# Kernel optimization log

Measured on AMD Instinct MI355X. Metric: run time of the kernel, lower is better.

Reference implementation:

```python
import jax, jax.numpy as jnp
import numpy as np
from jax import lax

B = 32; C_IN = 3; HW = 64
CL1_F = 64; CL1_K = 5
V = 1024
CL2_F = 128; CL2_K = 16
CL3_F = 256; CL3_K = 16
FC1_F = 512; FC2_F = 10
FC1_IN = CL3_F * (V // 16)  # 16384


def _sym_laplacian(k, v):
    # symmetric, spectral norm < 1 (mimics rescaled Laplacian 2L/lmax - I spectrum)
    a = jax.random.normal(k, (v, v), jnp.float32) / np.float32(np.sqrt(v))
    return (a + a.T) * jnp.float32(0.3)


def setup_inputs():
    key = jax.random.key(0)
    ks = jax.random.split(key, 10)
    def n(k, shape, s):
        return jax.random.normal(k, shape, jnp.float32) * jnp.float32(s)
    x = jax.random.normal(ks[0], (B, C_IN, HW, HW), jnp.float32)
    conv1_w = n(ks[1], (CL1_F, C_IN, CL1_K, CL1_K), 0.05)
    conv1_b = jnp.zeros((CL1_F,), jnp.float32)
    L1 = _sym_laplacian(ks[2], V)
    L2 = _sym_laplacian(ks[3], V // 4)
    g = HW // 2  # pooled grid side = 32
    ii, jj = jnp.meshgrid(jnp.arange(g), jnp.arange(g), indexing='ij')
    node_index = jnp.stack([ii.reshape(-1), jj.reshape(-1)], axis=1).astype(jnp.int32)  # [V,2]
    perm = jnp.arange(V, dtype=jnp.int32)
    k2_w = n(ks[4], (CL2_F, CL1_F * CL2_K), 0.04)
    k2_b = jnp.zeros((CL2_F,), jnp.float32)
    k3_w = n(ks[5], (CL3_F, CL2_F * CL3_K), 0.03)
    k3_b = jnp.zeros((CL3_F,), jnp.float32)
    fc1_w = n(ks[6], (FC1_F, FC1_IN), 0.01)
    fc1_b = jnp.zeros((FC1_F,), jnp.float32)
    fc2_w = n(ks[7], (FC2_F, FC1_F), 0.05)
    fc2_b = jnp.zeros((FC2_F,), jnp.float32)
    return {"x": x, "conv1_w": conv1_w, "conv1_b": conv1_b, "L1": L1, "L2": L2,
            "node_index": node_index, "perm": perm,
            "k2_w": k2_w, "k2_b": k2_b, "k3_w": k3_w, "k3_b": k3_b,
            "fc1_w": fc1_w, "fc1_b": fc1_b, "fc2_w": fc2_w, "fc2_b": fc2_b}


def _graph_conv(x, L, W, b, K):
    # x: (B, C, V). Chebyshev basis T_k(L) x, then linear over (C*K).
    Bb, C, Vv = x.shape
    x0 = jnp.transpose(x, (2, 1, 0)).reshape(Vv, C * Bb)  # [V, C*B]
    xs = [x0, L @ x0]
    for _ in range(K - 2):
        xs.append(2.0 * (L @ xs[-1]) - xs[-2])
    xk = jnp.stack(xs, axis=0).reshape(K, Vv, C, Bb)  # [K,V,C,B]
    xk = jnp.transpose(xk, (3, 1, 2, 0)).reshape(Bb * Vv, C * K)  # [B*V, C*K]
    out = xk @ W.T + b  # [B*V, Fout]
    return jnp.transpose(out.reshape(Bb, Vv, -1), (0, 2, 1))  # (B, Fout, V)


def reference(x, conv1_w, conv1_b, L1, L2, node_index, perm,
              k2_w, k2_b, k3_w, k3_b, fc1_w, fc1_b, fc2_w, fc2_b):
    pad = (CL1_K - 1) // 2
    y = lax.conv_general_dilated(x, conv1_w, (1, 1), [(pad, pad), (pad, pad)],
                                 dimension_numbers=('NCHW', 'OIHW', 'NCHW'))
    y = jax.nn.relu(y + conv1_b[None, :, None, None])
    Bb, C, H, Wd = y.shape
    y = y.reshape(Bb, C, H // 2, 2, Wd // 2, 2).max(axis=(3, 5))  # MaxPool2d(2,2)
    y = y[:, :, node_index[:, 0], node_index[:, 1]]  # (B, C, V)
    y = y[:, :, perm]
    # BatchNorm1d(affine=False), training-mode batch stats, biased variance
    mean = y.mean(axis=(0, 2), keepdims=True)
    var = y.var(axis=(0, 2), keepdims=True)
    y = (y - mean) * lax.rsqrt(var + 1e-5)
    y = jax.nn.relu(_graph_conv(y, L1, k2_w, k2_b, CL2_K))
    y = y.reshape(Bb, CL2_F, -1, 4).max(axis=-1)  # Graph_MaxPool(4)
    y = jax.nn.relu(_graph_conv(y, L2, k3_w, k3_b, CL3_K))
    y = y.reshape(Bb, CL3_F, -1, 4).max(axis=-1)
    y = y.reshape(Bb, FC1_IN)
    y = jax.nn.relu(y @ fc1_w.T + fc1_b)  # dropout p=0 -> identity
    return y @ fc2_w.T + fc2_b
```

## Files before the change

### kernel.cpp

```cpp
#include <hip/hip_runtime.h>
#include <hip/hip_bf16.h>

#define BB 32
#define C_IN 3
#define HW 64
#define V1 1024
#define CL2_F 128
#define V2 256
#define CL3_F 256
#define FC1_IN 16384

typedef unsigned short ushortT;
typedef __attribute__((ext_vector_type(8))) short bf16x8;
typedef __attribute__((ext_vector_type(8))) unsigned short u16x8;
typedef __attribute__((ext_vector_type(4))) float f32x4;

__device__ __forceinline__ float bfu2f(unsigned short u) {
  union { unsigned int i; float f; } x; x.i = ((unsigned)u) << 16; return x.f;
}
__device__ __forceinline__ unsigned short f2bf(float v) {
  union { float f; unsigned int i; } x; x.f = v;
  unsigned r = x.i + 0x7FFFu + ((x.i >> 16) & 1u);
  return (unsigned short)(r >> 16);
}
__device__ __forceinline__ void gload16(const ushortT* g, ushortT* l) {
  __builtin_amdgcn_global_load_lds((const __attribute__((address_space(1))) void*)g,
                                   (__attribute__((address_space(3))) void*)l, 16, 0, 0);
}

__global__ __launch_bounds__(256) void conv_pool_k(const float* __restrict__ x,
                                                   const float* __restrict__ w,
                                                   const float* __restrict__ bias,
                                                   float* __restrict__ P) {
  __shared__ float xs[3][7][72];
  __shared__ float wl[64][76];
  const int b = blockIdx.x >> 5, ph = blockIdx.x & 31;
  const int t = threadIdx.x;
  for (int i = t; i < 64 * 75; i += 256) wl[i / 75][i % 75] = w[i];
  for (int i = t; i < 3 * 7 * 72; i += 256) {
    int col = i % 72, rr = (i / 72) % 7, ci = i / (72 * 7);
    int ih = 2 * ph - 2 + rr, iw = col - 2;
    float v = 0.f;
    if (ih >= 0 && ih < HW && iw >= 0 && iw < HW)
      v = x[((b * 3 + ci) * HW + ih) * HW + iw];
    xs[ci][rr][col] = v;
  }
  __syncthreads();
  const int co = t >> 2, pq = t & 3;
  float acc[8][2][2];
#pragma unroll
  for (int i = 0; i < 8; ++i)
#pragma unroll
    for (int a = 0; a < 2; ++a)
#pragma unroll
      for (int d = 0; d < 2; ++d) acc[i][a][d] = 0.f;
  for (int ci = 0; ci < 3; ++ci) {
#pragma unroll
    for (int kh = 0; kh < 5; ++kh) {
      float w5[5];
#pragma unroll
      for (int j = 0; j < 5; ++j) w5[j] = wl[co][ci * 25 + kh * 5 + j];
#pragma unroll
      for (int dy = 0; dy < 2; ++dy) {
        const int r = kh + dy;
        float in[20];
#pragma unroll
        for (int q4 = 0; q4 < 5; ++q4) {
          float4 v4 = *(const float4*)&xs[ci][r][16 * pq + q4 * 4];
          in[q4 * 4 + 0] = v4.x; in[q4 * 4 + 1] = v4.y;
          in[q4 * 4 + 2] = v4.z; in[q4 * 4 + 3] = v4.w;
        }
#pragma unroll
        for (int i = 0; i < 8; ++i)
#pragma unroll
          for (int dx = 0; dx < 2; ++dx)
#pragma unroll
            for (int kw = 0; kw < 5; ++kw)
              acc[i][dy][dx] += w5[kw] * in[2 * i + dx + kw];
      }
    }
  }
  const float bv = bias[co];
#pragma unroll
  for (int i = 0; i < 8; ++i) {
    float m = fmaxf(fmaxf(acc[i][0][0], acc[i][0][1]), fmaxf(acc[i][1][0], acc[i][1][1]));
    P[((size_t)(b * 64 + co) << 10) + (ph << 5) + pq * 8 + i] = fmaxf(m + bv, 0.f);
  }
}

__global__ __launch_bounds__(256) void bn_part_k(const float* __restrict__ P,
                                                 float* __restrict__ buf) {
  int c = blockIdx.x, s = blockIdx.y;
  float s1 = 0.f, s2 = 0.f;
  for (int i = threadIdx.x; i < 4096; i += 256) {
    int b = s * 4 + (i >> 10), p = i & 1023;
    float v = P[((size_t)(b * 64 + c) << 10) + p];
    s1 += v; s2 += v * v;
  }
#pragma unroll
  for (int o = 32; o > 0; o >>= 1) { s1 += __shfl_down(s1, o); s2 += __shfl_down(s2, o); }
  __shared__ float sh[2][4];
  int wid = threadIdx.x >> 6;
  if ((threadIdx.x & 63) == 0) { sh[0][wid] = s1; sh[1][wid] = s2; }
  __syncthreads();
  if (threadIdx.x == 0) {
    buf[c * 8 + s] = sh[0][0] + sh[0][1] + sh[0][2] + sh[0][3];
    buf[512 + c * 8 + s] = sh[1][0] + sh[1][1] + sh[1][2] + sh[1][3];
  }
}
__global__ __launch_bounds__(64) void bn_comb_k(float* __restrict__ buf) {
  int c = threadIdx.x;
  float s1 = 0.f, s2 = 0.f;
#pragma unroll
  for (int s = 0; s < 8; ++s) { s1 += buf[c * 8 + s]; s2 += buf[512 + c * 8 + s]; }
  float mean = s1 / 32768.f;
  float var = s2 / 32768.f - mean * mean;
  buf[1024 + c] = mean;
  buf[1088 + c] = rsqrtf(var + 1e-5f);
}

__global__ __launch_bounds__(256) void build_x0_k(const float* __restrict__ P,
                                                  const float* __restrict__ buf,
                                                  const int* __restrict__ ni,
                                                  const int* __restrict__ perm,
                                                  ushortT* __restrict__ PGh,
                                                  ushortT* __restrict__ PGl,
                                                  ushortT* __restrict__ CW0) {
  __shared__ float vals[64][33];
  __shared__ int qv[32];
  const int b = blockIdx.x >> 5, vc = blockIdx.x & 31;
  const int t = threadIdx.x;
  if (t < 32) {
    int pv = perm[vc * 32 + t];
    qv[t] = ni[2 * pv] * 32 + ni[2 * pv + 1];
  }
  __syncthreads();
  {
    int c = t & 63, vh = t >> 6;
    float mean = buf[1024 + c], rstd = buf[1088 + c];
    const float* pc = &P[((size_t)(b * 64 + c)) << 10];
#pragma unroll
    for (int j = 0; j < 8; ++j) {
      int vl = vh * 8 + j;
      vals[c][vl] = (pc[qv[vl]] - mean) * rstd;
    }
  }
  __syncthreads();
  {
    int c = t & 63, vo = t >> 6;
    u16x8 h8, l8;
#pragma unroll
    for (int j = 0; j < 8; ++j) {
      float f = vals[c][vo * 8 + j];
      unsigned short h = f2bf(f);
      h8[j] = h; l8[j] = f2bf(f - bfu2f(h));
    }
    size_t base = ((size_t)(vc * 4 + vo) * 2048 + b * 64 + c) * 8;
    *(u16x8*)&PGh[base] = h8;
    *(u16x8*)&PGl[base] = l8;
  }
  {
    int co = t & 7, vl = t >> 3;
    u16x8 h8;
#pragma unroll
    for (int j = 0; j < 8; ++j) h8[j] = f2bf(vals[co * 8 + j][vl]);
    *(u16x8*)&CW0[((size_t)co * 32768 + b * 1024 + vc * 32 + vl) * 8] = h8;
  }
}

__global__ __launch_bounds__(256) void lsplit_k(const float* __restrict__ L,
                                                ushortT* __restrict__ Lh,
                                                ushortT* __restrict__ Ll, int V) {
  int id = blockIdx.x * 256 + threadIdx.x;
  int n = id & (V - 1), koct = id / V * 8;
  u16x8 h8, l8;
#pragma unroll
  for (int j = 0; j < 8; ++j) {
    float v = L[(size_t)(koct + j) * V + n];
    unsigned short h = f2bf(v);
    h8[j] = h; l8[j] = f2bf(v - bfu2f(h));
  }
  size_t o = (size_t)id * 8;
  *(u16x8*)&Lh[o] = h8;
  *(u16x8*)&Ll[o] = l8;
}

__global__ __launch_bounds__(256) void wprep_k(const float* __restrict__ W,
                                               ushortT* __restrict__ WAh,
                                               ushortT* __restrict__ WAl, int Cc, int Nf) {
  int d = blockIdx.x * 256 + threadIdx.x;
  if (d >= Nf * 16 * Cc) return;
  int c = d % Cc, kq = (d / Cc) % 16, f = d / (16 * Cc);
  float v = W[(size_t)f * (Cc * 16) + c * 16 + kq];
  unsigned short h = f2bf(v);
  WAh[d] = h; WAl[d] = f2bf(v - bfu2f(h));
}

template <int MODE, int SWZ, int KD>
__global__ __launch_bounds__(256) void cheb_step_k(
    int Mld, int mt,
    const ushortT* __restrict__ Ah, const ushortT* __restrict__ Al,
    const ushortT* __restrict__ Lbh, const ushortT* __restrict__ Lbl,
    ushortT* __restrict__ Ph, ushortT* __restrict__ Pl,
    ushortT* __restrict__ CW, int CB, int CSH) {
  __shared__ ushortT sA[2][2][8][520];
  int bx, by;
  if (SWZ) {
    const int id = blockIdx.x;
    const int xcd = id & 7, pos = id >> 3;
    bx = (xcd & 3) * 8 + (pos & 7);
    by = (xcd >> 2) * 8 + (pos >> 3);
  } else {
    bx = blockIdx.x % mt;
    by = blockIdx.x / mt;
  }
  const int m0 = bx * 64, n0 = by * 64;
  const int t = threadIdx.x, lane = t & 63;
  const int wr = (t >> 6) >> 1, wc = (t >> 6) & 1;
  const int lm = lane & 15, lq = lane >> 4;
  const size_t bCol = (size_t)(n0 + wc * 32 + lm);

  f32x4 acc[2][2];
#pragma unroll
  for (int mi = 0; mi < 2; ++mi)
#pragma unroll
    for (int nj = 0; nj < 2; ++nj) acc[mi][nj] = (f32x4){0.f, 0.f, 0.f, 0.f};

  bf16x8 B0h[2][2], B0l[2][2], B1h[2][2], B1l[2][2];

#define STAGEA(buf, k0)                                                            \
  {                                                                                \
    const int koct = (k0) >> 3;                                                    \
    _Pragma("unroll") for (int i = 0; i < 2; ++i) {                                \
      const int slot = (t + i * 256) >> 6;                                         \
      const int ln = t & 63;                                                       \
      const size_t ga = ((size_t)(koct + slot) * Mld + m0 + ln) * 8;               \
      gload16(Ah + ga, &sA[buf][0][slot][0]);                                      \
      gload16(Al + ga, &sA[buf][1][slot][0]);                                      \
    }                                                                              \
  }

#define LOADB(Bh_, Bl_, k0)                                                        \
  {                                                                                \
    _Pragma("unroll") for (int ks = 0; ks < 2; ++ks)                               \
        _Pragma("unroll") for (int nj = 0; nj < 2; ++nj) {                         \
      size_t o = ((size_t)(((k0) >> 3) + ks * 4 + lq) * KD + bCol + nj * 16) * 8;  \
      Bh_[ks][nj] = *(const bf16x8*)(Lbh + o);                                     \
      Bl_[ks][nj] = *(const bf16x8*)(Lbl + o);                                     \
    }                                                                              \
  }

#define DOMFMA(Bh_, Bl_, cur)                                                      \
  {                                                                                \
    _Pragma("unroll") for (int ks = 0; ks < 2; ++ks) {                             \
      const int so = ks * 4 + lq;                                                  \
      bf16x8 xah[2], xal[2];                                                       \
      _Pragma("unroll") for (int mi = 0; mi < 2; ++mi) {                           \
        const int r = (wr * 32 + mi * 16 + lm) * 8;                                \
        xah[mi] = *(const bf16x8*)&sA[cur][0][so][r];                              \
        xal[mi] = *(const bf16x8*)&sA[cur][1][so][r];                              \
      }                                                                            \
      _Pragma("unroll") for (int mi = 0; mi < 2; ++mi)                             \
          _Pragma("unroll") for (int nj = 0; nj < 2; ++nj) {                       \
        acc[mi][nj] = __builtin_amdgcn_mfma_f32_16x16x32_bf16(xah[mi], Bh_[ks][nj],\
                                                              acc[mi][nj], 0, 0, 0);\
        acc[mi][nj] = __builtin_amdgcn_mfma_f32_16x16x32_bf16(xal[mi], Bh_[ks][nj],\
                                                              acc[mi][nj], 0, 0, 0);\
        acc[mi][nj] = __builtin_amdgcn_mfma_f32_16x16x32_bf16(xah[mi], Bl_[ks][nj],\
                                                              acc[mi][nj], 0, 0, 0);\
      }                                                                            \
    }                                                                              \
  }

  STAGEA(0, 0);
  LOADB(B0h, B0l, 0);
  __syncthreads();
#pragma unroll
  for (int k0 = 0; k0 < KD; k0 += 128) {
    STAGEA(1, k0 + 64);
    LOADB(B1h, B1l, k0 + 64);
    DOMFMA(B0h, B0l, 0);
    __syncthreads();
    if (k0 + 128 < KD) {
      STAGEA(0, k0 + 128);
      LOADB(B0h, B0l, k0 + 128);
    }
    DOMFMA(B1h, B1l, 1);
    __syncthreads();
  }
#undef STAGEA
#undef LOADB
#undef DOMFMA

  float* fs = (float*)&sA[0][0][0][0];
#pragma unroll
  for (int mi = 0; mi < 2; ++mi)
#pragma unroll
    for (int nj = 0; nj < 2; ++nj)
#pragma unroll
      for (int j = 0; j < 4; ++j) {
        int gm_l = wr * 32 + mi * 16 + lq * 4 + j;
        int gn_l = wc * 32 + nj * 16 + lm;
        fs[gm_l * 65 + gn_l] = acc[mi][nj][j];
      }
  __syncthreads();

  const size_t noct0 = (size_t)(n0 >> 3);
#pragma unroll
  for (int r = 0; r < 2; ++r) {
    int id = t + r * 256;
    int gm_l = id >> 3, go = id & 7;
    size_t g = ((noct0 + go) * Mld + (m0 + gm_l)) * 8;
    float nv[8];
#pragma unroll
    for (int i = 0; i < 8; ++i) nv[i] = fs[gm_l * 65 + go * 8 + i];
    if (MODE == 1) {
      u16x8 ph = *(const u16x8*)&Ph[g];
      u16x8 pl = *(const u16x8*)&Pl[g];
#pragma unroll
      for (int i = 0; i < 8; ++i) nv[i] = 2.f * nv[i] - (bfu2f(ph[i]) + bfu2f(pl[i]));
    }
    u16x8 h8, l8;
#pragma unroll
    for (int i = 0; i < 8; ++i) {
      unsigned short h = f2bf(nv[i]);
      h8[i] = h; l8[i] = f2bf(nv[i] - bfu2f(h));
    }
    *(u16x8*)&Ph[g] = h8;
    *(u16x8*)&Pl[g] = l8;
    if (MODE == 1) {
#pragma unroll
      for (int i = 0; i < 8; ++i) fs[gm_l * 65 + go * 8 + i] = nv[i];
    }
  }
  __syncthreads();

  const int cBase = m0 & (CB - 1);
  const int bidx = m0 >> CSH;
  const size_t NNs = (size_t)KD << 5;
#pragma unroll
  for (int r = 0; r < 2; ++r) {
    int id = t + r * 256;
    int gn_l = id & 63, coI = id >> 6;
    u16x8 h8;
#pragma unroll
    for (int i = 0; i < 8; ++i) h8[i] = f2bf(fs[(coI * 8 + i) * 65 + gn_l]);
    size_t cbase = ((size_t)((cBase >> 3) + coI) * NNs + (size_t)bidx * KD + n0 + gn_l) * 8;
    *(u16x8*)&CW[cbase] = h8;
  }
}

template <int Cc, int NSPL>
__global__ __launch_bounds__(256) void wapply_k(
    int NN, int ldw,
    const ushortT* __restrict__ WAh, const ushortT* __restrict__ WAl,
    const ushortT* __restrict__ cwBase, size_t cwN,
    float* __restrict__ OUT, size_t outStride) {
  constexpr int S = Cc / 2;
  constexpr int SPZ = S / NSPL;
  const int z = blockIdx.z;
  OUT += (size_t)z * outStride;
  const int m0 = blockIdx.x * 64, n0 = blockIdx.y * 128;
  const int t = threadIdx.x, lane = t & 63, wid = t >> 6;
  const int wr = wid >> 1, wc = wid & 1;
  const int lm = lane & 15, lq = lane >> 4;

  const size_t wBase = (size_t)(m0 + wr * 32 + lm) * ldw + lq * 8;
  const int nb = n0 + wc * 64 + lm;
  const int s0 = z * SPZ;

  f32x4 acc[2][4];
#pragma unroll
  for (int mi = 0; mi < 2; ++mi)
#pragma unroll
    for (int nj = 0; nj < 4; ++nj) acc[mi][nj] = (f32x4){0.f, 0.f, 0.f, 0.f};

  bf16x8 wh[2][2], wl[2][2], xf[2][4];

#define LOADWX(b, s)                                                               \
  {                                                                                \
    const int buf_ = (Cc == 64) ? ((s) >> 1) : ((s) >> 2);                         \
    const int lo_ = (Cc == 64) ? (((s) & 1) * 4) : (((s) & 3) * 4);                \
    const ushortT* xb_ = cwBase + (size_t)buf_ * cwN;                              \
    _Pragma("unroll") for (int mi = 0; mi < 2; ++mi) {                             \
      size_t o = wBase + (size_t)(s)*32 + (size_t)mi * 16 * ldw;                   \
      wh[b][mi] = *(const bf16x8*)(WAh + o);                                       \
      wl[b][mi] = *(const bf16x8*)(WAl + o);                                       \
    }                                                                              \
    _Pragma("unroll") for (int nj = 0; nj < 4; ++nj)                               \
        xf[b][nj] = *(const bf16x8*)(xb_ + ((size_t)(lo_ + lq) * NN + nb + nj * 16) * 8); \
  }

  LOADWX(0, s0);
#pragma unroll
  for (int i = 0; i < SPZ; ++i) {
    if (i + 1 < SPZ) LOADWX((i + 1) & 1, s0 + i + 1);
    const int c_ = i & 1;
#pragma unroll
    for (int mi = 0; mi < 2; ++mi)
#pragma unroll
      for (int nj = 0; nj < 4; ++nj) {
        acc[mi][nj] = __builtin_amdgcn_mfma_f32_16x16x32_bf16(wh[c_][mi], xf[c_][nj], acc[mi][nj], 0, 0, 0);
        acc[mi][nj] = __builtin_amdgcn_mfma_f32_16x16x32_bf16(wl[c_][mi], xf[c_][nj], acc[mi][nj], 0, 0, 0);
      }
  }
#undef LOADWX

#pragma unroll
  for (int mi = 0; mi < 2; ++mi)
#pragma unroll
    for (int nj = 0; nj < 4; ++nj)
#pragma unroll
      for (int j = 0; j < 4; ++j) {
        int gm = m0 + wr * 32 + mi * 16 + lq * 4 + j;
        int gn = n0 + wc * 64 + nj * 16 + lm;
        OUT[(size_t)gm * NN + gn] = acc[mi][nj][j];
      }
}

__global__ __launch_bounds__(256) void relu_pool1_k(const float* __restrict__ OUT1P,
                                                    const float* __restrict__ b2,
                                                    ushortT* __restrict__ PG2h,
                                                    ushortT* __restrict__ PG2l,
                                                    ushortT* __restrict__ CW0) {
  __shared__ float sval[128][9];
  const int b = blockIdx.x >> 5, vc = blockIdx.x & 31;
  const int t = threadIdx.x;
  const size_t PS = (size_t)128 * 32768;
  {
    int f = t & 127, h = t >> 7;
    float bb = b2[f];
    const float* src = &OUT1P[(size_t)f * 32768 + b * 1024 + vc * 32];
#pragma unroll
    for (int i = 0; i < 4; ++i) {
      int v2l = h * 4 + i;
      float4 r0 = *(const float4*)&src[v2l * 4];
      float4 r1 = *(const float4*)&src[PS + v2l * 4];
      float s0 = r0.x + r1.x, s1 = r0.y + r1.y, s2 = r0.z + r1.z, s3 = r0.w + r1.w;
      float m = fmaxf(fmaxf(s0, s1), fmaxf(s2, s3));
      sval[f][v2l] = fmaxf(m + bb, 0.f);
    }
  }
  __syncthreads();
  if (t < 128) {
    int f = t;
    u16x8 h8, l8;
#pragma unroll
    for (int j = 0; j < 8; ++j) {
      float v = sval[f][j];
      unsigned short h = f2bf(v);
      h8[j] = h; l8[j] = f2bf(v - bfu2f(h));
    }
    size_t base = ((size_t)vc * 4096 + b * 128 + f) * 8;
    *(u16x8*)&PG2h[base] = h8;
    *(u16x8*)&PG2l[base] = l8;
  } else {
    int q = t - 128;
    int co = q & 15, v2l = q >> 4;
    u16x8 h8;
#pragma unroll
    for (int j = 0; j < 8; ++j) h8[j] = f2bf(sval[co * 8 + j][v2l]);
    *(u16x8*)&CW0[((size_t)co * 8192 + b * 256 + vc * 8 + v2l) * 8] = h8;
  }
}

__global__ __launch_bounds__(256) void relu_pool2_k(const float* __restrict__ OUT2P,
                                                    const float* __restrict__ b3,
                                                    float* __restrict__ At) {
  int n = blockIdx.x * 256 + threadIdx.x;
  int v3 = n & 63, f = (n >> 6) & 255, b = n >> 14;
  const size_t PS = (size_t)256 * 8192;
  size_t base = ((size_t)f * 32 + b) * 256 + v3 * 4;
  float4 r0 = *(const float4*)&OUT2P[base];
  float4 r1 = *(const float4*)&OUT2P[PS + base];
  float4 r2 = *(const float4*)&OUT2P[2 * PS + base];
  float4 r3 = *(const float4*)&OUT2P[3 * PS + base];
  float s0 = r0.x + r1.x + r2.x + r3.x;
  float s1 = r0.y + r1.y + r2.y + r3.y;
  float s2 = r0.z + r1.z + r2.z + r3.z;
  float s3 = r0.w + r1.w + r2.w + r3.w;
  float m = fmaxf(fmaxf(s0, s1), fmaxf(s2, s3));
  At[(size_t)b * FC1_IN + f * 64 + v3] = fmaxf(m + b3[f], 0.f);
}

__global__ __launch_bounds__(256) void fc1_part_k(const float* __restrict__ At,
                                                  const float* __restrict__ W1,
                                                  float* __restrict__ part) {
  __shared__ float sWt[64][68];
  __shared__ float sA[64][33];
  const int jt = blockIdx.x, ks = blockIdx.y;
  const int j0 = jt * 64, kb = ks * 512;
  const int t = threadIdx.x;
  const int b = t & 31, jg = t >> 5;
  float acc[8] = {};
  for (int k0 = kb; k0 < kb + 512; k0 += 64) {
    __syncthreads();
    {
      int jr = t >> 2, kq = t & 3;
      const float* wp = &W1[(size_t)(j0 + jr) * FC1_IN + k0 + kq * 16];
#pragma unroll
      for (int i = 0; i < 4; ++i) {
        float4 w4 = *(const float4*)(wp + 4 * i);
        int kk = kq * 16 + 4 * i;
        sWt[kk + 0][jr] = w4.x; sWt[kk + 1][jr] = w4.y;
        sWt[kk + 2][jr] = w4.z; sWt[kk + 3][jr] = w4.w;
      }
    }
    {
      int br = t >> 3, ko = t & 7;
      const float* ap = &At[(size_t)br * FC1_IN + k0 + ko * 8];
      float4 a0 = *(const float4*)ap;
      float4 a1 = *(const float4*)(ap + 4);
      int kk = ko * 8;
      sA[kk + 0][br] = a0.x; sA[kk + 1][br] = a0.y; sA[kk + 2][br] = a0.z; sA[kk + 3][br] = a0.w;
      sA[kk + 4][br] = a1.x; sA[kk + 5][br] = a1.y; sA[kk + 6][br] = a1.z; sA[kk + 7][br] = a1.w;
    }
    __syncthreads();
#pragma unroll 8
    for (int kk = 0; kk < 64; ++kk) {
      float a = sA[kk][b];
      float wv[8];
      *(float4*)wv = *(const float4*)&sWt[kk][jg * 8];
      *(float4*)(wv + 4) = *(const float4*)&sWt[kk][jg * 8 + 4];
#pragma unroll
      for (int i = 0; i < 8; ++i) acc[i] += wv[i] * a;
    }
  }
#pragma unroll
  for (int i = 0; i < 8; ++i)
    part[((size_t)ks * 512 + j0 + jg * 8 + i) * 32 + b] = acc[i];
}

__global__ __launch_bounds__(256) void fc1_combine_k(const float* __restrict__ part,
                                                     const float* __restrict__ b1,
                                                     float* __restrict__ h) {
  int n = blockIdx.x * 256 + threadIdx.x;
  int b = n >> 9, j = n & 511;
  float s = b1[j];
#pragma unroll
  for (int ks = 0; ks < 32; ++ks) s += part[((size_t)ks * 512 + j) * 32 + b];
  h[n] = fmaxf(s, 0.f);
}

__global__ __launch_bounds__(64) void fc2_k(const float* __restrict__ h,
                                            const float* __restrict__ W2,
                                            const float* __restrict__ b2f,
                                            float* __restrict__ out) {
  int n = blockIdx.x * 64 + threadIdx.x;
  if (n >= 320) return;
  int b = n / 10, o = n % 10;
  float s = b2f[o];
  const float* hp = h + b * 512;
  const float* wp = W2 + o * 512;
  for (int j = 0; j < 512; ++j) s += hp[j] * wp[j];
  out[n] = s;
}

extern "C" void kernel_launch(void* const* d_in, const int* in_sizes, int n_in,
                              void* d_out, int out_size, void* d_ws, size_t ws_size,
                              hipStream_t stream) {
  const float* x      = (const float*)d_in[0];
  const float* conv1w = (const float*)d_in[1];
  const float* conv1b = (const float*)d_in[2];
  const float* L1     = (const float*)d_in[3];
  const float* L2     = (const float*)d_in[4];
  const int*   ni     = (const int*)d_in[5];
  const int*   perm   = (const int*)d_in[6];
  const float* k2w    = (const float*)d_in[7];
  const float* k2b    = (const float*)d_in[8];
  const float* k3w    = (const float*)d_in[9];
  const float* k3b    = (const float*)d_in[10];
  const float* fc1w   = (const float*)d_in[11];
  const float* fc1b   = (const float*)d_in[12];
  const float* fc2w   = (const float*)d_in[13];
  const float* fc2b   = (const float*)d_in[14];
  float* out = (float*)d_out;

  char* ws = (char*)d_ws;
  const size_t MB = 1024 * 1024;
  float*   P    = (float*)(ws + 0);
  ushortT* cw1  = (ushortT*)(ws + 8 * MB);
  const size_t CW1N = 2u * 1024 * 1024;
  ushortT* pgAh = (ushortT*)(ws + 72 * MB);
  ushortT* pgAl = (ushortT*)(ws + 76 * MB);
  ushortT* pgBh = (ushortT*)(ws + 80 * MB);
  ushortT* pgBl = (ushortT*)(ws + 84 * MB);
  float*   OUT1P = (float*)(ws + 88 * MB);
  ushortT* L1h  = (ushortT*)(ws + 121 * MB);
  ushortT* L1l  = (ushortT*)(ws + 123 * MB);
  ushortT* WA1h = (ushortT*)(ws + 125 * MB);
  ushortT* WA1l = (ushortT*)(ws + 125 * MB + 262144);
  float*   BNB  = (float*)(ws + 126 * MB);
  ushortT* cw2  = (ushortT*)(ws + 0);
  const size_t CW2N = 1024u * 1024;
  ushortT* pg2Ah = (ushortT*)(ws + 32 * MB);
  ushortT* pg2Al = (ushortT*)(ws + 34 * MB);
  ushortT* pg2Bh = (ushortT*)(ws + 36 * MB);
  ushortT* pg2Bl = (ushortT*)(ws + 38 * MB);
  float*   OUT2P = (float*)(ws + 40 * MB);
  ushortT* L2h  = (ushortT*)(ws + 73 * MB);
  ushortT* L2l  = (ushortT*)(ws + 73 * MB + 131072);
  ushortT* WA2h = (ushortT*)(ws + 74 * MB);
  ushortT* WA2l = (ushortT*)(ws + 75 * MB);
  float*   At   = (float*)(ws + 76 * MB);
  float*   PART = (float*)(ws + 78 * MB);
  float*   H    = (float*)(ws + 80 * MB);

  conv_pool_k<<<1024, 256, 0, stream>>>(x, conv1w, conv1b, P);
  bn_part_k<<<dim3(64, 8), 256, 0, stream>>>(P, BNB);
  bn_comb_k<<<1, 64, 0, stream>>>(BNB);
  lsplit_k<<<512, 256, 0, stream>>>(L1, L1h, L1l, 1024);
  wprep_k<<<512, 256, 0, stream>>>(k2w, WA1h, WA1l, 64, 128);
  build_x0_k<<<1024, 256, 0, stream>>>(P, BNB, ni, perm, pgAh, pgAl, cw1 + 0 * CW1N);

  cheb_step_k<0, 1, 1024><<<512, 256, 0, stream>>>(2048, 32, pgAh, pgAl, L1h, L1l,
                                                   pgBh, pgBl, cw1 + 1 * CW1N, 64, 6);
  for (int k = 2; k < 16; ++k) {
    ushortT *ah, *al, *oh, *ol;
    if (k & 1) { ah = pgAh; al = pgAl; oh = pgBh; ol = pgBl; }
    else       { ah = pgBh; al = pgBl; oh = pgAh; ol = pgAl; }
    cheb_step_k<1, 1, 1024><<<512, 256, 0, stream>>>(2048, 32, ah, al, L1h, L1l,
                                                     oh, ol, cw1 + (size_t)k * CW1N, 64, 6);
  }
  wapply_k<64, 2><<<dim3(2, 256, 2), 256, 0, stream>>>(32768, 1024, WA1h, WA1l,
                                                       cw1, CW1N, OUT1P, (size_t)128 * 32768);

  relu_pool1_k<<<1024, 256, 0, stream>>>(OUT1P, k2b, pg2Ah, pg2Al, cw2 + 0 * CW2N);
  lsplit_k<<<32, 256, 0, stream>>>(L2, L2h, L2l, 256);
  wprep_k<<<2048, 256, 0, stream>>>(k3w, WA2h, WA2l, 128, 256);

  cheb_step_k<0, 0, 256><<<256, 256, 0, stream>>>(4096, 64, pg2Ah, pg2Al, L2h, L2l,
                                                  pg2Bh, pg2Bl, cw2 + 1 * CW2N, 128, 7);
  for (int k = 2; k < 16; ++k) {
    ushortT *ah, *al, *oh, *ol;
    if (k & 1) { ah = pg2Ah; al = pg2Al; oh = pg2Bh; ol = pg2Bl; }
    else       { ah = pg2Bh; al = pg2Bl; oh = pg2Ah; ol = pg2Al; }
    cheb_step_k<1, 0, 256><<<256, 256, 0, stream>>>(4096, 64, ah, al, L2h, L2l,
                                                    oh, ol, cw2 + (size_t)k * CW2N, 128, 7);
  }
  wapply_k<128, 4><<<dim3(4, 64, 4), 256, 0, stream>>>(8192, 2048, WA2h, WA2l,
                                                       cw2, CW2N, OUT2P, (size_t)256 * 8192);

  relu_pool2_k<<<2048, 256, 0, stream>>>(OUT2P, k3b, At);
  fc1_part_k<<<dim3(8, 32), 256, 0, stream>>>(At, fc1w, PART);
  fc1_combine_k<<<64, 256, 0, stream>>>(PART, fc1b, H);
  fc2_k<<<5, 64, 0, stream>>>(H, fc2w, fc2b, out);
}
```

Baseline: 577.2 us.

## Triple-buffer LDS pipelines in Chebyshev and weight-apply GEMMs, relayout weights

The Chebyshev step kernel moves from a double-buffered shared-memory loop with two full barriers per iteration to a three-stage ring. It uses explicit vmcnt waits, a single barrier per phase and raised wave priority around the MFMA block. The weight-apply kernel now stages its activation tiles through a three-deep LDS ring instead of reading them straight from global memory, and the weight prep writes an octet-major layout so weight fragments load contiguously. The aim is to hide global-load latency behind matrix math and cut barrier stalls. In exchange the code depends on hand-tuned waitcnt values, wraps loads modulo the phase count, and uses more LDS.

```diff
diff --git a/kernel.cpp b/kernel.cpp
--- a/kernel.cpp
+++ b/kernel.cpp
@@ -190,7 +190,11 @@
                                                ushortT* __restrict__ WAl, int Cc, int Nf) {
   int d = blockIdx.x * 256 + threadIdx.x;
   if (d >= Nf * 16 * Cc) return;
-  int c = d % Cc, kq = (d / Cc) % 16, f = d / (16 * Cc);
+  int j = d & 7;
+  int f = (d >> 3) % Nf;
+  int koct = d / (8 * Nf);
+  int k = koct * 8 + j;
+  int kq = k / Cc, c = k % Cc;
   float v = W[(size_t)f * (Cc * 16) + c * 16 + kq];
   unsigned short h = f2bf(v);
   WAh[d] = h; WAl[d] = f2bf(v - bfu2f(h));
@@ -203,7 +207,8 @@
     const ushortT* __restrict__ Lbh, const ushortT* __restrict__ Lbl,
     ushortT* __restrict__ Ph, ushortT* __restrict__ Pl,
     ushortT* __restrict__ CW, int CB, int CSH) {
-  __shared__ ushortT sA[2][2][8][520];
+  constexpr int NPH = KD / 64;
+  __shared__ ushortT sA[3][2][8][520];
   int bx, by;
   if (SWZ) {
     const int id = blockIdx.x;
@@ -226,68 +231,67 @@
 #pragma unroll
     for (int nj = 0; nj < 2; ++nj) acc[mi][nj] = (f32x4){0.f, 0.f, 0.f, 0.f};
 
-  bf16x8 B0h[2][2], B0l[2][2], B1h[2][2], B1l[2][2];
-
-#define STAGEA(buf, k0)                                                            \
+  bf16x8 Bh[2][2][2], Bl[2][2][2];
+
+#define STAGEA(buf, slot)                                                          \
   {                                                                                \
-    const int koct = (k0) >> 3;                                                    \
+    const int koct = (slot) * 8;                                                   \
     _Pragma("unroll") for (int i = 0; i < 2; ++i) {                                \
-      const int slot = (t + i * 256) >> 6;                                         \
+      const int sl = (t + i * 256) >> 6;                                           \
       const int ln = t & 63;                                                       \
-      const size_t ga = ((size_t)(koct + slot) * Mld + m0 + ln) * 8;               \
-      gload16(Ah + ga, &sA[buf][0][slot][0]);                                      \
-      gload16(Al + ga, &sA[buf][1][slot][0]);                                      \
+      const size_t ga = ((size_t)(koct + sl) * Mld + m0 + ln) * 8;                 \
+      gload16(Ah + ga, &sA[buf][0][sl][0]);                                        \
+      gload16(Al + ga, &sA[buf][1][sl][0]);                                        \
     }                                                                              \
   }
 
-#define LOADB(Bh_, Bl_, k0)                                                        \
+#define LOADB(set, slot)                                                           \
   {                                                                                \
     _Pragma("unroll") for (int ks = 0; ks < 2; ++ks)                               \
         _Pragma("unroll") for (int nj = 0; nj < 2; ++nj) {                         \
-      size_t o = ((size_t)(((k0) >> 3) + ks * 4 + lq) * KD + bCol + nj * 16) * 8;  \
-      Bh_[ks][nj] = *(const bf16x8*)(Lbh + o);                                     \
-      Bl_[ks][nj] = *(const bf16x8*)(Lbl + o);                                     \
+      size_t o = ((size_t)((slot) * 8 + ks * 4 + lq) * KD + bCol + nj * 16) * 8;   \
+      Bh[set][ks][nj] = *(const bf16x8*)(Lbh + o);                                 \
+      Bl[set][ks][nj] = *(const bf16x8*)(Lbl + o);                                 \
     }                                                                              \
   }
 
-#define DOMFMA(Bh_, Bl_, cur)                                                      \
+#define DOMFMA(buf, set)                                                           \
   {                                                                                \
     _Pragma("unroll") for (int ks = 0; ks < 2; ++ks) {                             \
       const int so = ks * 4 + lq;                                                  \
       bf16x8 xah[2], xal[2];                                                       \
       _Pragma("unroll") for (int mi = 0; mi < 2; ++mi) {                           \
         const int r = (wr * 32 + mi * 16 + lm) * 8;                                \
-        xah[mi] = *(const bf16x8*)&sA[cur][0][so][r];                              \
-        xal[mi] = *(const bf16x8*)&sA[cur][1][so][r];                              \
+        xah[mi] = *(const bf16x8*)&sA[buf][0][so][r];                              \
+        xal[mi] = *(const bf16x8*)&sA[buf][1][so][r];                              \
       }                                                                            \
       _Pragma("unroll") for (int mi = 0; mi < 2; ++mi)                             \
           _Pragma("unroll") for (int nj = 0; nj < 2; ++nj) {                       \
-        acc[mi][nj] = __builtin_amdgcn_mfma_f32_16x16x32_bf16(xah[mi], Bh_[ks][nj],\
+        acc[mi][nj] = __builtin_amdgcn_mfma_f32_16x16x32_bf16(xah[mi], Bh[set][ks][nj], \
                                                               acc[mi][nj], 0, 0, 0);\
-        acc[mi][nj] = __builtin_amdgcn_mfma_f32_16x16x32_bf16(xal[mi], Bh_[ks][nj],\
+        acc[mi][nj] = __builtin_amdgcn_mfma_f32_16x16x32_bf16(xal[mi], Bh[set][ks][nj], \
                                                               acc[mi][nj], 0, 0, 0);\
-        acc[mi][nj] = __builtin_amdgcn_mfma_f32_16x16x32_bf16(xah[mi], Bl_[ks][nj],\
+        acc[mi][nj] = __builtin_amdgcn_mfma_f32_16x16x32_bf16(xah[mi], Bl[set][ks][nj], \
                                                               acc[mi][nj], 0, 0, 0);\
       }                                                                            \
     }                                                                              \
   }
 
   STAGEA(0, 0);
-  LOADB(B0h, B0l, 0);
-  __syncthreads();
-#pragma unroll
-  for (int k0 = 0; k0 < KD; k0 += 128) {
-    STAGEA(1, k0 + 64);
-    LOADB(B1h, B1l, k0 + 64);
-    DOMFMA(B0h, B0l, 0);
-    __syncthreads();
-    if (k0 + 128 < KD) {
-      STAGEA(0, k0 + 128);
-      LOADB(B0h, B0l, k0 + 128);
-    }
-    DOMFMA(B1h, B1l, 1);
-    __syncthreads();
-  }
+  STAGEA(1, 1);
+  LOADB(0, 0);
+#pragma unroll
+  for (int tt = 0; tt < NPH; ++tt) {
+    asm volatile("s_waitcnt vmcnt(12) lgkmcnt(0)" ::: "memory");
+    __builtin_amdgcn_s_barrier();
+    STAGEA((tt + 2) % 3, (tt + 2) % NPH);
+    LOADB((tt + 1) % 2, (tt + 1) % NPH);
+    __builtin_amdgcn_s_setprio(1);
+    DOMFMA(tt % 3, tt % 2);
+    __builtin_amdgcn_s_setprio(0);
+  }
+  asm volatile("s_waitcnt vmcnt(0)" ::: "memory");
+  __syncthreads();
 #undef STAGEA
 #undef LOADB
 #undef DOMFMA
@@ -352,12 +356,14 @@
 
 template <int Cc, int NSPL>
 __global__ __launch_bounds__(256) void wapply_k(
-    int NN, int ldw,
+    int NN, int Nf,
     const ushortT* __restrict__ WAh, const ushortT* __restrict__ WAl,
     const ushortT* __restrict__ cwBase, size_t cwN,
     float* __restrict__ OUT, size_t outStride) {
   constexpr int S = Cc / 2;
   constexpr int SPZ = S / NSPL;
+  constexpr int ROWU = 129 * 8;
+  __shared__ ushortT sX[3][4 * ROWU];
   const int z = blockIdx.z;
   OUT += (size_t)z * outStride;
   const int m0 = blockIdx.x * 64, n0 = blockIdx.y * 128;
@@ -365,8 +371,7 @@
   const int wr = wid >> 1, wc = wid & 1;
   const int lm = lane & 15, lq = lane >> 4;
 
-  const size_t wBase = (size_t)(m0 + wr * 32 + lm) * ldw + lq * 8;
-  const int nb = n0 + wc * 64 + lm;
+  const int fIdx = m0 + wr * 32 + lm;
   const int s0 = z * SPZ;
 
   f32x4 acc[2][4];
@@ -375,36 +380,61 @@
 #pragma unroll
     for (int nj = 0; nj < 4; ++nj) acc[mi][nj] = (f32x4){0.f, 0.f, 0.f, 0.f};
 
-  bf16x8 wh[2][2], wl[2][2], xf[2][4];
-
-#define LOADWX(b, s)                                                               \
+  bf16x8 wh[2][2], wl[2][2];
+
+#define STX(buf, s)                                                                \
   {                                                                                \
     const int buf_ = (Cc == 64) ? ((s) >> 1) : ((s) >> 2);                         \
     const int lo_ = (Cc == 64) ? (((s) & 1) * 4) : (((s) & 3) * 4);                \
     const ushortT* xb_ = cwBase + (size_t)buf_ * cwN;                              \
+    _Pragma("unroll") for (int i = 0; i < 2; ++i) {                                \
+      const int idx = t + i * 256;                                                 \
+      const int octrow = idx >> 7, col = idx & 127;                                \
+      const int chunk = idx >> 6;                                                  \
+      const ushortT* src = xb_ + ((size_t)(lo_ + octrow) * NN + n0 + col) * 8;     \
+      gload16(src, &sX[buf][octrow * ROWU + (chunk & 1) * 512]);                   \
+    }                                                                              \
+  }
+
+#define LDW(set, s)                                                                \
+  {                                                                                \
     _Pragma("unroll") for (int mi = 0; mi < 2; ++mi) {                             \
-      size_t o = wBase + (size_t)(s)*32 + (size_t)mi * 16 * ldw;                   \
-      wh[b][mi] = *(const bf16x8*)(WAh + o);                                       \
-      wl[b][mi] = *(const bf16x8*)(WAl + o);                                       \
+      size_t o = ((size_t)((s)*4 + lq) * Nf + fIdx + mi * 16) * 8;                 \
+      wh[set][mi] = *(const bf16x8*)(WAh + o);                                     \
+      wl[set][mi] = *(const bf16x8*)(WAl + o);                                     \
     }                                                                              \
+  }
+
+#define XMFMA(buf, set)                                                            \
+  {                                                                                \
+    bf16x8 xf[4];                                                                  \
     _Pragma("unroll") for (int nj = 0; nj < 4; ++nj)                               \
-        xf[b][nj] = *(const bf16x8*)(xb_ + ((size_t)(lo_ + lq) * NN + nb + nj * 16) * 8); \
-  }
-
-  LOADWX(0, s0);
-#pragma unroll
-  for (int i = 0; i < SPZ; ++i) {
-    if (i + 1 < SPZ) LOADWX((i + 1) & 1, s0 + i + 1);
-    const int c_ = i & 1;
-#pragma unroll
-    for (int mi = 0; mi < 2; ++mi)
-#pragma unroll
-      for (int nj = 0; nj < 4; ++nj) {
-        acc[mi][nj] = __builtin_amdgcn_mfma_f32_16x16x32_bf16(wh[c_][mi], xf[c_][nj], acc[mi][nj], 0, 0, 0);
-        acc[mi][nj] = __builtin_amdgcn_mfma_f32_16x16x32_bf16(wl[c_][mi], xf[c_][nj], acc[mi][nj], 0, 0, 0);
-      }
-  }
-#undef LOADWX
+        xf[nj] = *(const bf16x8*)&sX[buf][lq * ROWU + (wc * 64 + lm + nj * 16) * 8];\
+    _Pragma("unroll") for (int mi = 0; mi < 2; ++mi)                               \
+        _Pragma("unroll") for (int nj = 0; nj < 4; ++nj) {                         \
+      acc[mi][nj] = __builtin_amdgcn_mfma_f32_16x16x32_bf16(wh[set][mi], xf[nj],   \
+                                                            acc[mi][nj], 0, 0, 0); \
+      acc[mi][nj] = __builtin_amdgcn_mfma_f32_16x16x32_bf16(wl[set][mi], xf[nj],   \
+                                                            acc[mi][nj], 0, 0, 0); \
+    }                                                                              \
+  }
+
+  STX(0, s0);
+  STX(1, s0 + 1);
+  LDW(0, s0);
+#pragma unroll
+  for (int tt = 0; tt < SPZ; ++tt) {
+    asm volatile("s_waitcnt vmcnt(6) lgkmcnt(0)" ::: "memory");
+    __builtin_amdgcn_s_barrier();
+    STX((tt + 2) % 3, s0 + (tt + 2) % SPZ);
+    LDW((tt + 1) % 2, s0 + (tt + 1) % SPZ);
+    __builtin_amdgcn_s_setprio(1);
+    XMFMA(tt % 3, tt % 2);
+    __builtin_amdgcn_s_setprio(0);
+  }
+#undef STX
+#undef LDW
+#undef XMFMA
 
 #pragma unroll
   for (int mi = 0; mi < 2; ++mi)
@@ -622,7 +652,7 @@
     cheb_step_k<1, 1, 1024><<<512, 256, 0, stream>>>(2048, 32, ah, al, L1h, L1l,
                                                      oh, ol, cw1 + (size_t)k * CW1N, 64, 6);
   }
-  wapply_k<64, 2><<<dim3(2, 256, 2), 256, 0, stream>>>(32768, 1024, WA1h, WA1l,
+  wapply_k<64, 2><<<dim3(2, 256, 2), 256, 0, stream>>>(32768, 128, WA1h, WA1l,
                                                        cw1, CW1N, OUT1P, (size_t)128 * 32768);
 
   relu_pool1_k<<<1024, 256, 0, stream>>>(OUT1P, k2b, pg2Ah, pg2Al, cw2 + 0 * CW2N);
@@ -638,7 +668,7 @@
     cheb_step_k<1, 0, 256><<<256, 256, 0, stream>>>(4096, 64, ah, al, L2h, L2l,
                                                     oh, ol, cw2 + (size_t)k * CW2N, 128, 7);
   }
-  wapply_k<128, 4><<<dim3(4, 64, 4), 256, 0, stream>>>(8192, 2048, WA2h, WA2l,
+  wapply_k<128, 4><<<dim3(4, 64, 4), 256, 0, stream>>>(8192, 256, WA2h, WA2l,
                                                        cw2, CW2N, OUT2P, (size_t)256 * 8192);
 
   relu_pool2_k<<<2048, 256, 0, stream>>>(OUT2P, k3b, At);
```

After: 570.7 us. About the same (-1.1%).
